# Kernel tuning notes

Hardware: AMD Instinct MI355X
Metric: run time of the kernel (lower is better)

## Reference

```python
import jax, jax.numpy as jnp
import numpy as np


def setup_inputs() -> dict:
    key = jax.random.key(0)
    k1, k2 = jax.random.split(key)
    p_hat = jax.random.normal(k1, (16384, 3), dtype=jnp.float32)
    p = jax.random.normal(k2, (16384, 3), dtype=jnp.float32)
    return {"p_hat": p_hat, "p": p}


def reference(p_hat, p):
    # squared pairwise L2 distances: ||a-b||^2 = ||a||^2 + ||b||^2 - 2 a.b
    a2 = jnp.sum(p_hat * p_hat, axis=-1)            # [N]
    b2 = jnp.sum(p * p, axis=-1)                    # [M]
    cross = p_hat @ p.T                             # [N, M]
    d2 = jnp.maximum(a2[:, None] + b2[None, :] - 2.0 * cross, 0.0)
    # Chamfer: mean of col-mins (min over dim 0) + mean of row-mins (min over dim 1)
    return jnp.mean(jnp.min(d2, axis=0)) + jnp.mean(jnp.min(d2, axis=1))
```

## Files before the change

### kernel.cpp

```cpp
#include <hip/hip_runtime.h>
#include <hip/hip_bf16.h>

#define N 16384
#define TPB 256
#define QPT 4
#define QTILE (TPB * QPT)
#define NQT (N / QTILE)
#define SPLIT 64
#define CHUNK (N / SPLIT)
#define GRID (2 * SPLIT * NQT)
#define INF_BITS 0x7F800000

__global__ void pack_kernel(const float* __restrict__ p_hat,
                            const float* __restrict__ p,
                            float4* __restrict__ q4,
                            int* __restrict__ minbuf) {
    int idx = blockIdx.x * blockDim.x + threadIdx.x;
    if (idx >= 2 * N) return;
    const float* src = (idx < N) ? p_hat : p;
    int k = (idx < N) ? idx : idx - N;
    float x = src[3 * k + 0], y = src[3 * k + 1], z = src[3 * k + 2];
    q4[idx] = make_float4(x, y, z, x * x + y * y + z * z);
    minbuf[idx] = INF_BITS;
}

__global__ void __launch_bounds__(TPB) chamfer_kernel(const float4* __restrict__ q4,
                                                      int* __restrict__ minbuf) {
    int b    = blockIdx.x;
    int dir  = b & 1;
    int rest = b >> 1;
    int jc   = rest & (SPLIT - 1);
    int qt   = rest >> 6;

    const float4* __restrict__ qp = q4 + (dir ? N : 0);
    const float4* __restrict__ rp = q4 + (dir ? 0 : N);

    int ibase = qt * QTILE + (int)threadIdx.x;
    float m2x[QPT], m2y[QPT], m2z[QPT], qw[QPT], vmin[QPT];
#pragma unroll
    for (int q = 0; q < QPT; ++q) {
        float4 qq = qp[ibase + q * TPB];
        m2x[q] = -2.0f * qq.x; m2y[q] = -2.0f * qq.y; m2z[q] = -2.0f * qq.z;
        qw[q] = qq.w;
        vmin[q] = __builtin_inff();
    }

    int j0 = j0 = jc * CHUNK;
    float4 ra = rp[j0];
    float4 rb = rp[j0 + 1];
#pragma unroll 2
    for (int j = j0; j < j0 + CHUNK; j += 2) {
        float4 na = rp[j + 2];
        float4 nb = rp[j + 3];
        float raw = ra.w, rbw = rb.w;
#pragma unroll
        for (int q = 0; q < QPT; ++q) {
            float ta = __builtin_fmaf(ra.x, m2x[q],
                       __builtin_fmaf(ra.y, m2y[q],
                       __builtin_fmaf(ra.z, m2z[q], raw)));
            float tb = __builtin_fmaf(rb.x, m2x[q],
                       __builtin_fmaf(rb.y, m2y[q],
                       __builtin_fmaf(rb.z, m2z[q], rbw)));
            asm("v_min3_f32 %0, %0, %1, %2" : "+v"(vmin[q]) : "v"(ta), "v"(tb));
        }
        ra = na; rb = nb;
    }

#pragma unroll
    for (int q = 0; q < QPT; ++q) {
        float m = fmaxf(vmin[q] + qw[q], 0.0f);
        atomicMin(&minbuf[dir * N + ibase + q * TPB], __float_as_int(m));
    }
}

__global__ void __launch_bounds__(1024) reduce_kernel(const int* __restrict__ minbuf,
                                                      float* __restrict__ out) {
    const int4* mb4 = (const int4*)minbuf;
    float s = 0.0f;
#pragma unroll
    for (int k = 0; k < (2 * N / 4) / 1024; ++k) {
        int4 v = mb4[k * 1024 + threadIdx.x];
        s += __int_as_float(v.x) + __int_as_float(v.y) +
             __int_as_float(v.z) + __int_as_float(v.w);
    }
    for (int off = 32; off > 0; off >>= 1) s += __shfl_down(s, off, 64);
    __shared__ float partial[1024 / 64];
    int lane = threadIdx.x & 63;
    int wid  = threadIdx.x >> 6;
    if (lane == 0) partial[wid] = s;
    __syncthreads();
    if (threadIdx.x == 0) {
        float t = 0.0f;
        for (int w = 0; w < 1024 / 64; ++w) t += partial[w];
        out[0] = t / (float)N;
    }
}

extern "C" void kernel_launch(void* const* d_in, const int* in_sizes, int n_in,
                              void* d_out, int out_size, void* d_ws, size_t ws_size,
                              hipStream_t stream) {
    const float* p_hat = (const float*)d_in[0];
    const float* p     = (const float*)d_in[1];
    float4* q4     = (float4*)d_ws;
    int*    minbuf = (int*)((char*)d_ws + 2 * N * sizeof(float4));
    float*  out    = (float*)d_out;

    pack_kernel<<<(2 * N + TPB - 1) / TPB, TPB, 0, stream>>>(p_hat, p, q4, minbuf);
    chamfer_kernel<<<GRID, TPB, 0, stream>>>(q4, minbuf);
    reduce_kernel<<<1, 1024, 0, stream>>>(minbuf, out);
}
```

Before: 110.2 us.

## Compute chamfer distances with bf16 MFMA using hi/lo split operands

```diff
diff --git a/kernel.cpp b/kernel.cpp
--- a/kernel.cpp
+++ b/kernel.cpp
@@ -1,75 +1,130 @@
 #include <hip/hip_runtime.h>
-#include <hip/hip_bf16.h>
 
 #define N 16384
 #define TPB 256
-#define QPT 4
-#define QTILE (TPB * QPT)
-#define NQT (N / QTILE)
-#define SPLIT 64
-#define CHUNK (N / SPLIT)
-#define GRID (2 * SPLIT * NQT)
 #define INF_BITS 0x7F800000
 
-__global__ void pack_kernel(const float* __restrict__ p_hat,
-                            const float* __restrict__ p,
-                            float4* __restrict__ q4,
-                            int* __restrict__ minbuf) {
+#define NT32 (N / 32)
+#define MT 2
+#define NSTRIP (NT32 / MT)
+#define NJSPLIT 8
+#define JW (NT32 / NJSPLIT)
+#define NBLK_MFMA (2 * NSTRIP * NJSPLIT / 4)
+#define FRAG_U4 (NT32 * 64)
+#define WS_NEED_MFMA (4ull * FRAG_U4 * sizeof(uint4) + 2ull * N * sizeof(int))
+
+using bf16x8 = __attribute__((ext_vector_type(8))) short;
+using fx16   = __attribute__((ext_vector_type(16))) float;
+
+__device__ __forceinline__ unsigned short bf16_rn(float f) {
+    unsigned u = __float_as_uint(f);
+    u += 0x7FFFu + ((u >> 16) & 1u);
+    return (unsigned short)(u >> 16);
+}
+__device__ __forceinline__ float bf16f(unsigned short h) {
+    return __uint_as_float(((unsigned)h) << 16);
+}
+__device__ __forceinline__ uint4 pack8(const unsigned short* a) {
+    return make_uint4((unsigned)a[0] | ((unsigned)a[1] << 16),
+                      (unsigned)a[2] | ((unsigned)a[3] << 16),
+                      (unsigned)a[4] | ((unsigned)a[5] << 16),
+                      (unsigned)a[6] | ((unsigned)a[7] << 16));
+}
+
+__global__ void pack_mfma(const float* __restrict__ p_hat, const float* __restrict__ p,
+                          uint4* __restrict__ frags, int* __restrict__ minbuf)
+{
     int idx = blockIdx.x * blockDim.x + threadIdx.x;
     if (idx >= 2 * N) return;
+    minbuf[idx] = INF_BITS;
     const float* src = (idx < N) ? p_hat : p;
-    int k = (idx < N) ? idx : idx - N;
-    float x = src[3 * k + 0], y = src[3 * k + 1], z = src[3 * k + 2];
-    q4[idx] = make_float4(x, y, z, x * x + y * y + z * z);
-    minbuf[idx] = INF_BITS;
-}
-
-__global__ void __launch_bounds__(TPB) chamfer_kernel(const float4* __restrict__ q4,
-                                                      int* __restrict__ minbuf) {
-    int b    = blockIdx.x;
-    int dir  = b & 1;
-    int rest = b >> 1;
-    int jc   = rest & (SPLIT - 1);
-    int qt   = rest >> 6;
-
-    const float4* __restrict__ qp = q4 + (dir ? N : 0);
-    const float4* __restrict__ rp = q4 + (dir ? 0 : N);
-
-    int ibase = qt * QTILE + (int)threadIdx.x;
-    float m2x[QPT], m2y[QPT], m2z[QPT], qw[QPT], vmin[QPT];
-#pragma unroll
-    for (int q = 0; q < QPT; ++q) {
-        float4 qq = qp[ibase + q * TPB];
-        m2x[q] = -2.0f * qq.x; m2y[q] = -2.0f * qq.y; m2z[q] = -2.0f * qq.z;
-        qw[q] = qq.w;
-        vmin[q] = __builtin_inff();
-    }
-
-    int j0 = j0 = jc * CHUNK;
-    float4 ra = rp[j0];
-    float4 rb = rp[j0 + 1];
-#pragma unroll 2
-    for (int j = j0; j < j0 + CHUNK; j += 2) {
-        float4 na = rp[j + 2];
-        float4 nb = rp[j + 3];
-        float raw = ra.w, rbw = rb.w;
-#pragma unroll
-        for (int q = 0; q < QPT; ++q) {
-            float ta = __builtin_fmaf(ra.x, m2x[q],
-                       __builtin_fmaf(ra.y, m2y[q],
-                       __builtin_fmaf(ra.z, m2z[q], raw)));
-            float tb = __builtin_fmaf(rb.x, m2x[q],
-                       __builtin_fmaf(rb.y, m2y[q],
-                       __builtin_fmaf(rb.z, m2z[q], rbw)));
-            asm("v_min3_f32 %0, %0, %1, %2" : "+v"(vmin[q]) : "v"(ta), "v"(tb));
+    int i = (idx < N) ? idx : idx - N;
+    float x = src[3*i+0], y = src[3*i+1], z = src[3*i+2];
+
+    unsigned short xh = bf16_rn(x), yh = bf16_rn(y), zh = bf16_rn(z);
+    unsigned short xl = bf16_rn(x - bf16f(xh));
+    unsigned short yl = bf16_rn(y - bf16f(yh));
+    unsigned short zl = bf16_rn(z - bf16f(zh));
+    float s = __builtin_fmaf(x, x, __builtin_fmaf(y, y, z * z));
+    unsigned short sh = bf16_rn(s), sl = bf16_rn(s - bf16f(sh));
+    unsigned short m2xh = bf16_rn(-2.0f * bf16f(xh)), m2xl = bf16_rn(-2.0f * bf16f(xl));
+    unsigned short m2yh = bf16_rn(-2.0f * bf16f(yh)), m2yl = bf16_rn(-2.0f * bf16f(yl));
+    unsigned short m2zh = bf16_rn(-2.0f * bf16f(zh)), m2zl = bf16_rn(-2.0f * bf16f(zl));
+    const unsigned short one = 0x3F80;
+
+    unsigned short q[16] = { m2xh, m2xh, m2xl, m2xl, m2yh, m2yh, m2yl, m2yl,
+                             m2zh, m2zh, m2zl, m2zl, sh, sl, one, one };
+    unsigned short r[16] = { xh, xl, xh, xl, yh, yl, yh, yl,
+                             zh, zl, zh, zl, one, one, sh, sl };
+
+    uint4* Qa = frags + ((idx < N) ? 0 : FRAG_U4);
+    uint4* Ra = frags + 2 * FRAG_U4 + ((idx < N) ? 0 : FRAG_U4);
+    int t = i >> 5, rr = i & 31;
+    Qa[t * 64 +      rr] = pack8(q);
+    Qa[t * 64 + 32 + rr] = pack8(q + 8);
+    Ra[t * 64 +      rr] = pack8(r);
+    Ra[t * 64 + 32 + rr] = pack8(r + 8);
+}
+
+__global__ void __launch_bounds__(TPB, 4) chamfer_mfma(const uint4* __restrict__ frags,
+                                                       int* __restrict__ minbuf)
+{
+    int lane = threadIdx.x & 63;
+    int wid  = blockIdx.x * 4 + (threadIdx.x >> 6);
+    int strip  = wid & (NSTRIP - 1);
+    int jsplit = (wid >> 8) & (NJSPLIT - 1);
+    int pass   = wid >> 11;
+
+    const uint4* Q = frags + (pass ? FRAG_U4 : 0);
+    const uint4* R = frags + 2 * FRAG_U4 + (pass ? 0 : FRAG_U4);
+
+    bf16x8 A[MT];
+#pragma unroll
+    for (int m = 0; m < MT; ++m) {
+        uint4 a = Q[(strip * MT + m) * 64 + lane];
+        A[m] = __builtin_bit_cast(bf16x8, a);
+    }
+    fx16 zf;
+#pragma unroll
+    for (int r2 = 0; r2 < 16; ++r2) zf[r2] = 0.0f;
+    fx16 rmin[MT];
+#pragma unroll
+    for (int m = 0; m < MT; ++m)
+#pragma unroll
+        for (int r2 = 0; r2 < 16; ++r2) rmin[m][r2] = __builtin_inff();
+
+    const uint4* Rj = R + jsplit * (JW * 64) + lane;
+    uint4 cur = Rj[0];
+    for (int jj = 0; jj < JW; ++jj) {
+        int nxt = (jj + 1 < JW) ? (jj + 1) : 0;
+        uint4 nx = Rj[nxt * 64];
+        bf16x8 B = __builtin_bit_cast(bf16x8, cur);
+#pragma unroll
+        for (int m = 0; m < MT; ++m) {
+            fx16 d = __builtin_amdgcn_mfma_f32_32x32x16_bf16(A[m], B, zf, 0, 0, 0);
+#pragma unroll
+            for (int r2 = 0; r2 < 16; ++r2)
+                rmin[m][r2] = fminf(rmin[m][r2], d[r2]);
         }
-        ra = na; rb = nb;
-    }
-
-#pragma unroll
-    for (int q = 0; q < QPT; ++q) {
-        float m = fmaxf(vmin[q] + qw[q], 0.0f);
-        atomicMin(&minbuf[dir * N + ibase + q * TPB], __float_as_int(m));
+        cur = nx;
+    }
+
+    int rowbase = pass * N + strip * (MT * 32) + 4 * (lane >> 5);
+#pragma unroll
+    for (int m = 0; m < MT; ++m) {
+#pragma unroll
+        for (int r2 = 0; r2 < 16; ++r2) {
+            float v = rmin[m][r2];
+            v = fminf(v, __shfl_xor(v, 1));
+            v = fminf(v, __shfl_xor(v, 2));
+            v = fminf(v, __shfl_xor(v, 4));
+            v = fminf(v, __shfl_xor(v, 8));
+            v = fminf(v, __shfl_xor(v, 16));
+            if ((lane & 31) == 0) {
+                int row = rowbase + m * 32 + (r2 & 3) + 8 * (r2 >> 2);
+                atomicMin(&minbuf[row], __float_as_int(fmaxf(v, 0.0f)));
+            }
+        }
     }
 }
 
@@ -96,16 +151,85 @@
     }
 }
 
+#define OQPT 4
+#define OQTILE (TPB * OQPT)
+#define ONQT (N / OQTILE)
+#define OSPLIT 64
+#define OCHUNK (N / OSPLIT)
+#define OGRID (2 * OSPLIT * ONQT)
+
+__global__ void pack_old(const float* __restrict__ p_hat, const float* __restrict__ p,
+                         float4* __restrict__ q4, int* __restrict__ minbuf) {
+    int idx = blockIdx.x * blockDim.x + threadIdx.x;
+    if (idx >= 2 * N) return;
+    const float* src = (idx < N) ? p_hat : p;
+    int k = (idx < N) ? idx : idx - N;
+    float x = src[3*k+0], y = src[3*k+1], z = src[3*k+2];
+    q4[idx] = make_float4(x, y, z, x*x + y*y + z*z);
+    minbuf[idx] = INF_BITS;
+}
+
+__global__ void __launch_bounds__(TPB) chamfer_old(const float4* __restrict__ q4,
+                                                   int* __restrict__ minbuf) {
+    int b = blockIdx.x;
+    int dir = b & 1;
+    int rest = b >> 1;
+    int jc = rest & (OSPLIT - 1);
+    int qt = rest >> 6;
+    const float4* __restrict__ qp = q4 + (dir ? N : 0);
+    const float4* __restrict__ rp = q4 + (dir ? 0 : N);
+    int ibase = qt * OQTILE + (int)threadIdx.x;
+    float m2x[OQPT], m2y[OQPT], m2z[OQPT], qw[OQPT], vmin[OQPT];
+#pragma unroll
+    for (int q = 0; q < OQPT; ++q) {
+        float4 qq = qp[ibase + q * TPB];
+        m2x[q] = -2.0f * qq.x; m2y[q] = -2.0f * qq.y; m2z[q] = -2.0f * qq.z;
+        qw[q] = qq.w; vmin[q] = __builtin_inff();
+    }
+    int j0 = jc * OCHUNK;
+    float4 ra = rp[j0];
+    float4 rb = rp[j0 + 1];
+#pragma unroll 2
+    for (int j = j0; j < j0 + OCHUNK; j += 2) {
+        float4 na = rp[j + 2];
+        float4 nb = rp[j + 3];
+        float raw = ra.w, rbw = rb.w;
+#pragma unroll
+        for (int q = 0; q < OQPT; ++q) {
+            float ta = __builtin_fmaf(ra.x, m2x[q],
+                       __builtin_fmaf(ra.y, m2y[q],
+                       __builtin_fmaf(ra.z, m2z[q], raw)));
+            float tb = __builtin_fmaf(rb.x, m2x[q],
+                       __builtin_fmaf(rb.y, m2y[q],
+                       __builtin_fmaf(rb.z, m2z[q], rbw)));
+            asm("v_min3_f32 %0, %0, %1, %2" : "+v"(vmin[q]) : "v"(ta), "v"(tb));
+        }
+        ra = na; rb = nb;
+    }
+#pragma unroll
+    for (int q = 0; q < OQPT; ++q) {
+        float m = fmaxf(vmin[q] + qw[q], 0.0f);
+        atomicMin(&minbuf[dir * N + ibase + q * TPB], __float_as_int(m));
+    }
+}
+
 extern "C" void kernel_launch(void* const* d_in, const int* in_sizes, int n_in,
                               void* d_out, int out_size, void* d_ws, size_t ws_size,
                               hipStream_t stream) {
     const float* p_hat = (const float*)d_in[0];
     const float* p     = (const float*)d_in[1];
-    float4* q4     = (float4*)d_ws;
-    int*    minbuf = (int*)((char*)d_ws + 2 * N * sizeof(float4));
-    float*  out    = (float*)d_out;
-
-    pack_kernel<<<(2 * N + TPB - 1) / TPB, TPB, 0, stream>>>(p_hat, p, q4, minbuf);
-    chamfer_kernel<<<GRID, TPB, 0, stream>>>(q4, minbuf);
-    reduce_kernel<<<1, 1024, 0, stream>>>(minbuf, out);
-}
+    float* out = (float*)d_out;
+    if (ws_size >= WS_NEED_MFMA) {
+        uint4* frags = (uint4*)d_ws;
+        int* minbuf  = (int*)((char*)d_ws + 4ull * FRAG_U4 * sizeof(uint4));
+        pack_mfma<<<(2 * N + TPB - 1) / TPB, TPB, 0, stream>>>(p_hat, p, frags, minbuf);
+        chamfer_mfma<<<NBLK_MFMA, TPB, 0, stream>>>(frags, minbuf);
+        reduce_kernel<<<1, 1024, 0, stream>>>(minbuf, out);
+    } else {
+        float4* q4  = (float4*)d_ws;
+        int* minbuf = (int*)((char*)d_ws + 2 * N * sizeof(float4));
+        pack_old<<<(2 * N + TPB - 1) / TPB, TPB, 0, stream>>>(p_hat, p, q4, minbuf);
+        chamfer_old<<<OGRID, TPB, 0, stream>>>(q4, minbuf);
+        reduce_kernel<<<1, 1024, 0, stream>>>(minbuf, out);
+    }
+}
```

Result: slower. 118.4 us (+7.5%).
